# Optimization experiments

Hardware: AMD Instinct MI355X
Metric: run time of the kernel (lower is better)

The kernel has to match this reference:

```python
import math
import jax, jax.numpy as jnp
import numpy as np

B, S, D, H = 2, 2048, 2048, 16
HD = D // H
SCALE = 1.0 / math.sqrt(HD)


def setup_inputs() -> dict:
    key = jax.random.key(0)
    kx, kq, kk, kv, ko = jax.random.split(key, 5)
    w_std = 1.0 / math.sqrt(D)
    return {
        "x": jax.random.normal(kx, (B, S, D), jnp.float32),
        "Wq": jax.random.normal(kq, (D, D), jnp.float32) * w_std,
        "Wk": jax.random.normal(kk, (D, D), jnp.float32) * w_std,
        "Wv": jax.random.normal(kv, (D, D), jnp.float32) * w_std,
        "Wo": jax.random.normal(ko, (D, D), jnp.float32) * w_std,
        "attention_mask": jnp.ones((B, S), jnp.int32),
        "sliding_window": 512,
        "sink_tokens": 4,
    }


def reference(x, Wq, Wk, Wv, Wo, attention_mask, sliding_window, sink_tokens):
    b, s, d = x.shape
    # nn.Linear(bias=False): y = x @ W^T
    q = (x @ Wq.T).reshape(b, s, H, HD).transpose(0, 2, 1, 3)  # [b,h,s,hd]
    k = (x @ Wk.T).reshape(b, s, H, HD).transpose(0, 2, 1, 3)
    v = (x @ Wv.T).reshape(b, s, H, HD).transpose(0, 2, 1, 3)

    scores = jnp.einsum("bhqd,bhkd->bhqk", q, k) * SCALE  # [b,h,s,s]

    i = jnp.arange(s)[:, None]
    j = jnp.arange(s)[None, :]
    causal = j <= i
    window = (j >= i - sliding_window + 1) & (j <= i)
    # sink mask in the source fills [0:i+1] for every row (rows < sink_tokens
    # and rows >= sink_tokens alike), i.e. it is identical to the causal mask.
    sink = causal
    allowed = causal & window & sink  # [s,s]
    pad = (attention_mask != 0)[:, None, None, :]  # [b,1,1,s]
    scores = jnp.where(allowed[None, None] & pad, scores, -jnp.inf)

    attn = jax.nn.softmax(scores, axis=-1)
    out = jnp.einsum("bhqk,bhkd->bhqd", attn, v)  # [b,h,s,hd]
    out = out.transpose(0, 2, 1, 3).reshape(b, s, d)
    return out @ Wo.T
```

## Files before the change

kernel.cpp:

```cpp
#include <hip/hip_runtime.h>
#include <stdint.h>


typedef __attribute__((ext_vector_type(8))) short short8;
typedef __attribute__((ext_vector_type(4))) float f32x4;

#define DEV static __device__ __forceinline__

DEV unsigned short f2bf(float f) {
  unsigned u = __builtin_bit_cast(unsigned, f);
  u += 0x7fffu + ((u >> 16) & 1u);
  return (unsigned short)(u >> 16);
}

DEV void async16(const void* g, void* l) {
  __builtin_amdgcn_global_load_lds(
      (const __attribute__((address_space(1))) unsigned int*)g,
      (__attribute__((address_space(3))) unsigned int*)l, 16, 0, 0);
}

__global__ void cast_bf16(const float* __restrict__ src,
                          unsigned short* __restrict__ dst, int n8) {
  int i = blockIdx.x * blockDim.x + threadIdx.x;
  if (i >= n8) return;
  const float4* s4 = (const float4*)src;
  float4 a = s4[2 * (size_t)i], b = s4[2 * (size_t)i + 1];
  short8 o;
  o[0] = (short)f2bf(a.x); o[1] = (short)f2bf(a.y);
  o[2] = (short)f2bf(a.z); o[3] = (short)f2bf(a.w);
  o[4] = (short)f2bf(b.x); o[5] = (short)f2bf(b.y);
  o[6] = (short)f2bf(b.z); o[7] = (short)f2bf(b.w);
  *(short8*)(dst + 8 * (size_t)i) = o;
}

constexpr int GK = 2048, GN = 2048;

template <bool STORE_BF16>
__global__ __launch_bounds__(256) void gemm_bt(
    const unsigned short* __restrict__ A, const unsigned short* __restrict__ B,
    void* __restrict__ Cout, size_t obuf_stride) {
  __shared__ short As[128 * 32];
  __shared__ short Bs[128 * 32];
  const int t = threadIdx.x;
  const int wave = t >> 6, lane = t & 63;
  const int row0 = blockIdx.x * 128;
  const int col0g = blockIdx.y * 128;
  const int nb = col0g >> 11, col0 = col0g & 2047;
  const int wrow = (wave >> 1) * 64, wcol = (wave & 1) * 64;

  f32x4 acc[4][4] = {};

  const int srow = wave * 16 + (lane >> 2);
  const int cg = (lane & 3) ^ (lane >> 4);
  const unsigned short* Ag0 = A + (size_t)(row0 + srow) * GK + cg * 8;
  const unsigned short* Ag1 = A + (size_t)(row0 + 64 + srow) * GK + cg * 8;
  const unsigned short* Bg0 = B + (size_t)(col0g + srow) * GK + cg * 8;
  const unsigned short* Bg1 = B + (size_t)(col0g + 64 + srow) * GK + cg * 8;
  char* lA0 = (char*)As + wave * 1024;
  char* lA1 = (char*)As + 4096 + wave * 1024;
  char* lB0 = (char*)Bs + wave * 1024;
  char* lB1 = (char*)Bs + 4096 + wave * 1024;

  const int quad = lane >> 4, l15 = lane & 15;
  const int cpos = quad ^ ((l15 >> 2) & 3);
  const short* ap[4];
  const short* bp[4];
#pragma unroll
  for (int i = 0; i < 4; ++i) {
    ap[i] = As + (wrow + i * 16 + l15) * 32 + cpos * 8;
    bp[i] = Bs + (wcol + i * 16 + l15) * 32 + cpos * 8;
  }

  for (int kk = 0; kk < GK; kk += 32) {
    async16(Ag0 + kk, lA0);
    async16(Ag1 + kk, lA1);
    async16(Bg0 + kk, lB0);
    async16(Bg1 + kk, lB1);
    __syncthreads();
    short8 af[4], bf[4];
#pragma unroll
    for (int i = 0; i < 4; ++i) af[i] = *(const short8*)ap[i];
#pragma unroll
    for (int i = 0; i < 4; ++i) bf[i] = *(const short8*)bp[i];
#pragma unroll
    for (int mi = 0; mi < 4; ++mi)
#pragma unroll
      for (int ni = 0; ni < 4; ++ni)
        acc[mi][ni] = __builtin_amdgcn_mfma_f32_16x16x32_bf16(
            af[mi], bf[ni], acc[mi][ni], 0, 0, 0);
    __syncthreads();
  }

#pragma unroll
  for (int mi = 0; mi < 4; ++mi)
#pragma unroll
    for (int ni = 0; ni < 4; ++ni)
#pragma unroll
      for (int r = 0; r < 4; ++r) {
        int row = row0 + wrow + mi * 16 + quad * 4 + r;
        int col = col0 + wcol + ni * 16 + l15;
        if (STORE_BF16)
          ((unsigned short*)Cout)[nb * obuf_stride + (size_t)row * GN + col] =
              f2bf(acc[mi][ni][r]);
        else
          ((float*)Cout)[nb * obuf_stride + (size_t)row * GN + col] =
              acc[mi][ni][r];
      }
}

__global__ __launch_bounds__(256) void transpose_v(
    const unsigned short* __restrict__ vb, unsigned short* __restrict__ vtb) {
  __shared__ unsigned short tile[64][72];
  const int s0 = blockIdx.x * 64, d0 = blockIdx.y * 64, b = blockIdx.z;
  const int tid = threadIdx.x;
  const int c8 = tid & 7;
#pragma unroll
  for (int i = 0; i < 2; ++i) {
    int row = i * 32 + (tid >> 3);
    uint4 v = *(const uint4*)(vb + (size_t)(b * 2048 + s0 + row) * 2048 + d0 + c8 * 8);
    *(uint4*)&tile[row][c8 * 8] = v;
  }
  __syncthreads();
#pragma unroll
  for (int i = 0; i < 2; ++i) {
    int dr = i * 32 + (tid >> 3);
    short8 sv;
#pragma unroll
    for (int j = 0; j < 8; ++j) sv[j] = (short)tile[c8 * 8 + j][dr];
    int d = d0 + dr;
    int h = d >> 7, hd = d & 127;
    *(short8*)(vtb + ((size_t)(b * 16 + h) * 128 + hd) * 2048 + s0 + c8 * 8) = sv;
  }
}

__global__ __launch_bounds__(256, 2) void attn_mfma(
    const unsigned short* __restrict__ Qm, const unsigned short* __restrict__ Km,
    const unsigned short* __restrict__ Vt, unsigned short* __restrict__ Om,
    const int* __restrict__ amask, const int* __restrict__ winp) {
  constexpr int S = 2048, D = 2048, HD = 128;
  const float SCALE = 0.08838834764831845f;

  __shared__ short Ks[64 * 128];
  __shared__ short Vts[128 * 64];
  __shared__ short Ps[4][2][16 * 64];

  const int t = threadIdx.x, w = t >> 6, lane = t & 63;
  const int quad = lane >> 4, l15 = lane & 15;
  const int l7 = l15 & 7;
  const int qt = blockIdx.x, h = blockIdx.y, b = blockIdx.z;
  const int qi0 = qt * 128;
  const int win = winp[0];

  short8 qf[2][4];
#pragma unroll
  for (int mi = 0; mi < 2; ++mi) {
    const unsigned short* qp =
        Qm + (size_t)(b * S + qi0 + w * 32 + mi * 16 + l15) * D + h * HD + quad * 8;
#pragma unroll
    for (int kc = 0; kc < 4; ++kc) qf[mi][kc] = *(const short8*)(qp + kc * 32);
  }

  f32x4 o[2][8] = {};
  float m_r[2][4], l_r[2][4];
#pragma unroll
  for (int mi = 0; mi < 2; ++mi)
#pragma unroll
    for (int r = 0; r < 4; ++r) { m_r[mi][r] = -1e30f; l_r[mi][r] = 0.f; }

  int lowj = qi0 - win + 1;
  if (lowj < 0) lowj = 0;
  const int jt0 = lowj >> 6, jt1 = 2 * qt + 1;

  const int gmin = qi0 + w * 32, gmax = gmin + 31;
  const int krow = lane >> 4, kpos = lane & 15;
  const int vrow = lane >> 3, vpos = lane & 7;

  for (int jt = jt0; jt <= jt1; ++jt) {
    const int j0 = jt * 64;
    __syncthreads();
#pragma unroll
    for (int ii = 0; ii < 4; ++ii) {
      int row = ii * 16 + w * 4 + krow;
      int c = kpos ^ (row & 7);
      async16(Km + (size_t)(b * S + j0 + row) * D + h * HD + c * 8,
              (char*)Ks + (ii * 16 + w * 4) * 256);
    }
#pragma unroll
    for (int ii = 0; ii < 4; ++ii) {
      int row = ii * 32 + w * 8 + vrow;
      int c = vpos ^ (row & 7);
      async16(Vt + ((size_t)(b * 16 + h) * 128 + row) * S + j0 + c * 8,
              (char*)Vts + (ii * 32 + w * 8) * 128);
    }
    __syncthreads();

    if (j0 > gmax || j0 + 63 < gmin - win + 1) continue;

    int amv[4];
#pragma unroll
    for (int ni = 0; ni < 4; ++ni) amv[ni] = amask[b * S + j0 + ni * 16 + l15];

    f32x4 sS[2][4];
#pragma unroll
    for (int ni = 0; ni < 4; ++ni) {
      f32x4 a0 = {0.f, 0.f, 0.f, 0.f}, a1 = {0.f, 0.f, 0.f, 0.f};
#pragma unroll
      for (int kc = 0; kc < 4; ++kc) {
        int pos = (kc * 4 + quad) ^ l7;
        short8 bk = *(const short8*)&Ks[(ni * 16 + l15) * 128 + pos * 8];
        a0 = __builtin_amdgcn_mfma_f32_16x16x32_bf16(qf[0][kc], bk, a0, 0, 0, 0);
        a1 = __builtin_amdgcn_mfma_f32_16x16x32_bf16(qf[1][kc], bk, a1, 0, 0, 0);
      }
      sS[0][ni] = a0;
      sS[1][ni] = a1;
    }

    float alpha[2][4];
#pragma unroll
    for (int mi = 0; mi < 2; ++mi) {
      float sv[4][4];
#pragma unroll
      for (int ni = 0; ni < 4; ++ni)
#pragma unroll
        for (int r = 0; r < 4; ++r) {
          int gi = qi0 + w * 32 + mi * 16 + quad * 4 + r;
          int gj = j0 + ni * 16 + l15;
          bool ok = (gj <= gi) && (gj >= gi - win + 1) && (amv[ni] != 0);
          sv[ni][r] = ok ? sS[mi][ni][r] * SCALE : -1e30f;
        }
      float mnew[4];
#pragma unroll
      for (int r = 0; r < 4; ++r) {
        float mx = fmaxf(fmaxf(sv[0][r], sv[1][r]), fmaxf(sv[2][r], sv[3][r]));
        mx = fmaxf(mx, __shfl_xor(mx, 1));
        mx = fmaxf(mx, __shfl_xor(mx, 2));
        mx = fmaxf(mx, __shfl_xor(mx, 4));
        mx = fmaxf(mx, __shfl_xor(mx, 8));
        float mn = fmaxf(m_r[mi][r], mx);
        alpha[mi][r] = __expf(m_r[mi][r] - mn);
        m_r[mi][r] = mn;
        mnew[r] = mn;
      }
      float rs[4] = {0.f, 0.f, 0.f, 0.f};
#pragma unroll
      for (int ni = 0; ni < 4; ++ni)
#pragma unroll
        for (int r = 0; r < 4; ++r) {
          float p = (sv[ni][r] > -1e29f) ? __expf(sv[ni][r] - mnew[r]) : 0.f;
          sv[ni][r] = p;
          rs[r] += p;
        }
#pragma unroll
      for (int r = 0; r < 4; ++r) {
        float s = rs[r];
        s += __shfl_xor(s, 1);
        s += __shfl_xor(s, 2);
        s += __shfl_xor(s, 4);
        s += __shfl_xor(s, 8);
        l_r[mi][r] = l_r[mi][r] * alpha[mi][r] + s;
      }
#pragma unroll
      for (int ni = 0; ni < 4; ++ni)
#pragma unroll
        for (int r = 0; r < 4; ++r) {
          int row = quad * 4 + r;
          int col = ni * 16 + l15;
          int pos = (col >> 3) ^ (row & 7);
          Ps[w][mi][row * 64 + pos * 8 + (col & 7)] = (short)f2bf(sv[ni][r]);
        }
    }
#pragma unroll
    for (int mi = 0; mi < 2; ++mi)
#pragma unroll
      for (int ni2 = 0; ni2 < 8; ++ni2)
#pragma unroll
        for (int r = 0; r < 4; ++r) o[mi][ni2][r] *= alpha[mi][r];

    __asm__ __volatile__("s_waitcnt lgkmcnt(0)" ::: "memory");

    short8 aP[2][2];
#pragma unroll
    for (int mi = 0; mi < 2; ++mi)
#pragma unroll
      for (int kc2 = 0; kc2 < 2; ++kc2) {
        int pos = (kc2 * 4 + quad) ^ l7;
        aP[mi][kc2] = *(const short8*)&Ps[w][mi][l15 * 64 + pos * 8];
      }
#pragma unroll
    for (int ni2 = 0; ni2 < 8; ++ni2)
#pragma unroll
      for (int kc2 = 0; kc2 < 2; ++kc2) {
        int pos = (kc2 * 4 + quad) ^ l7;
        short8 bv = *(const short8*)&Vts[(ni2 * 16 + l15) * 64 + pos * 8];
        o[0][ni2] = __builtin_amdgcn_mfma_f32_16x16x32_bf16(aP[0][kc2], bv,
                                                            o[0][ni2], 0, 0, 0);
        o[1][ni2] = __builtin_amdgcn_mfma_f32_16x16x32_bf16(aP[1][kc2], bv,
                                                            o[1][ni2], 0, 0, 0);
      }
  }

#pragma unroll
  for (int mi = 0; mi < 2; ++mi) {
    float inv[4];
#pragma unroll
    for (int r = 0; r < 4; ++r) inv[r] = 1.f / l_r[mi][r];
#pragma unroll
    for (int ni2 = 0; ni2 < 8; ++ni2)
#pragma unroll
      for (int r = 0; r < 4; ++r) {
        int row = qi0 + w * 32 + mi * 16 + quad * 4 + r;
        Om[(size_t)(b * S + row) * D + h * HD + ni2 * 16 + l15] =
            f2bf(o[mi][ni2][r] * inv[r]);
      }
  }
}

extern "C" void kernel_launch(void* const* d_in, const int* in_sizes, int n_in,
                              void* d_out, int out_size, void* d_ws,
                              size_t ws_size, hipStream_t stream) {
  (void)in_sizes; (void)n_in; (void)out_size; (void)ws_size;
  const float* x  = (const float*)d_in[0];
  const float* Wq = (const float*)d_in[1];
  const float* Wk = (const float*)d_in[2];
  const float* Wv = (const float*)d_in[3];
  const float* Wo = (const float*)d_in[4];
  const int* am   = (const int*)d_in[5];
  const int* win  = (const int*)d_in[6];

  char* ws = (char*)d_ws;
  unsigned short* xb   = (unsigned short*)(ws + 0);
  unsigned short* vtb  = (unsigned short*)(ws + 0);
  unsigned short* wqkv = (unsigned short*)(ws + 16777216);
  unsigned short* wob  = (unsigned short*)(ws + 41943040);
  unsigned short* qb   = (unsigned short*)(ws + 50331648);
  unsigned short* kb   = (unsigned short*)(ws + 67108864);
  unsigned short* vb   = (unsigned short*)(ws + 83886080);
  unsigned short* ab   = (unsigned short*)(ws + 100663296);

  cast_bf16<<<dim3(4096), dim3(256), 0, stream>>>(x, xb, 1048576);
  cast_bf16<<<dim3(2048), dim3(256), 0, stream>>>(Wq, wqkv, 524288);
  cast_bf16<<<dim3(2048), dim3(256), 0, stream>>>(Wk, wqkv + 4194304, 524288);
  cast_bf16<<<dim3(2048), dim3(256), 0, stream>>>(Wv, wqkv + 8388608, 524288);
  cast_bf16<<<dim3(2048), dim3(256), 0, stream>>>(Wo, wob, 524288);

  gemm_bt<true><<<dim3(32, 48), dim3(256), 0, stream>>>(xb, wqkv, qb, 8388608);

  transpose_v<<<dim3(32, 32, 2), dim3(256), 0, stream>>>(vb, vtb);

  attn_mfma<<<dim3(16, 16, 2), dim3(256), 0, stream>>>(qb, kb, vtb, ab, am, win);

  gemm_bt<false><<<dim3(32, 16), dim3(256), 0, stream>>>(ab, wob, d_out, 0);
}
```

Baseline: 378.6 us.

## Fuse cast kernels and split-K the output projection with atomics

Merges the five fp32-to-bf16 cast launches into a single kernel that picks its source and destination from the block index, cutting launch overhead. The output projection GEMM now splits K into two halves across blockIdx.z and accumulates into a zeroed fp32 output with atomicAdd, doubling the block count from 512 to 1024 to better fill the GPU. This adds a memset and atomic traffic, and the summation order becomes nondeterministic.

```diff
diff --git a/kernel.cpp b/kernel.cpp
--- a/kernel.cpp
+++ b/kernel.cpp
@@ -19,10 +19,26 @@
       (__attribute__((address_space(3))) unsigned int*)l, 16, 0, 0);
 }
 
-__global__ void cast_bf16(const float* __restrict__ src,
-                          unsigned short* __restrict__ dst, int n8) {
-  int i = blockIdx.x * blockDim.x + threadIdx.x;
-  if (i >= n8) return;
+__global__ __launch_bounds__(256) void cast_all(
+    const float* __restrict__ x, const float* __restrict__ Wq,
+    const float* __restrict__ Wk, const float* __restrict__ Wv,
+    const float* __restrict__ Wo, unsigned short* __restrict__ xb,
+    unsigned short* __restrict__ wqkv, unsigned short* __restrict__ wob) {
+  const int bid = blockIdx.x;
+  const float* src;
+  unsigned short* dst;
+  int i;
+  if (bid < 4096) {
+    src = x; dst = xb; i = bid * 256 + threadIdx.x;
+  } else if (bid < 6144) {
+    src = Wq; dst = wqkv; i = (bid - 4096) * 256 + threadIdx.x;
+  } else if (bid < 8192) {
+    src = Wk; dst = wqkv + 4194304; i = (bid - 6144) * 256 + threadIdx.x;
+  } else if (bid < 10240) {
+    src = Wv; dst = wqkv + 8388608; i = (bid - 8192) * 256 + threadIdx.x;
+  } else {
+    src = Wo; dst = wob; i = (bid - 10240) * 256 + threadIdx.x;
+  }
   const float4* s4 = (const float4*)src;
   float4 a = s4[2 * (size_t)i], b = s4[2 * (size_t)i + 1];
   short8 o;
@@ -35,10 +51,9 @@
 
 constexpr int GK = 2048, GN = 2048;
 
-template <bool STORE_BF16>
 __global__ __launch_bounds__(256) void gemm_bt(
     const unsigned short* __restrict__ A, const unsigned short* __restrict__ B,
-    void* __restrict__ Cout, size_t obuf_stride) {
+    unsigned short* __restrict__ Cout, size_t obuf_stride) {
   __shared__ short As[128 * 32];
   __shared__ short Bs[128 * 32];
   const int t = threadIdx.x;
@@ -99,12 +114,73 @@
       for (int r = 0; r < 4; ++r) {
         int row = row0 + wrow + mi * 16 + quad * 4 + r;
         int col = col0 + wcol + ni * 16 + l15;
-        if (STORE_BF16)
-          ((unsigned short*)Cout)[nb * obuf_stride + (size_t)row * GN + col] =
-              f2bf(acc[mi][ni][r]);
-        else
-          ((float*)Cout)[nb * obuf_stride + (size_t)row * GN + col] =
-              acc[mi][ni][r];
+        Cout[nb * obuf_stride + (size_t)row * GN + col] = f2bf(acc[mi][ni][r]);
+      }
+}
+
+__global__ __launch_bounds__(256) void gemm_sk(
+    const unsigned short* __restrict__ A, const unsigned short* __restrict__ B,
+    float* __restrict__ Cout) {
+  __shared__ short As[128 * 32];
+  __shared__ short Bs[128 * 32];
+  const int t = threadIdx.x;
+  const int wave = t >> 6, lane = t & 63;
+  const int row0 = blockIdx.x * 128, col0 = blockIdx.y * 128;
+  const int k0 = blockIdx.z * 1024;
+  const int wrow = (wave >> 1) * 64, wcol = (wave & 1) * 64;
+
+  f32x4 acc[4][4] = {};
+
+  const int srow = wave * 16 + (lane >> 2);
+  const int cg = (lane & 3) ^ (lane >> 4);
+  const unsigned short* Ag0 = A + (size_t)(row0 + srow) * GK + cg * 8;
+  const unsigned short* Ag1 = A + (size_t)(row0 + 64 + srow) * GK + cg * 8;
+  const unsigned short* Bg0 = B + (size_t)(col0 + srow) * GK + cg * 8;
+  const unsigned short* Bg1 = B + (size_t)(col0 + 64 + srow) * GK + cg * 8;
+  char* lA0 = (char*)As + wave * 1024;
+  char* lA1 = (char*)As + 4096 + wave * 1024;
+  char* lB0 = (char*)Bs + wave * 1024;
+  char* lB1 = (char*)Bs + 4096 + wave * 1024;
+
+  const int quad = lane >> 4, l15 = lane & 15;
+  const int cpos = quad ^ ((l15 >> 2) & 3);
+  const short* ap[4];
+  const short* bp[4];
+#pragma unroll
+  for (int i = 0; i < 4; ++i) {
+    ap[i] = As + (wrow + i * 16 + l15) * 32 + cpos * 8;
+    bp[i] = Bs + (wcol + i * 16 + l15) * 32 + cpos * 8;
+  }
+
+  for (int kk = k0; kk < k0 + 1024; kk += 32) {
+    async16(Ag0 + kk, lA0);
+    async16(Ag1 + kk, lA1);
+    async16(Bg0 + kk, lB0);
+    async16(Bg1 + kk, lB1);
+    __syncthreads();
+    short8 af[4], bf[4];
+#pragma unroll
+    for (int i = 0; i < 4; ++i) af[i] = *(const short8*)ap[i];
+#pragma unroll
+    for (int i = 0; i < 4; ++i) bf[i] = *(const short8*)bp[i];
+#pragma unroll
+    for (int mi = 0; mi < 4; ++mi)
+#pragma unroll
+      for (int ni = 0; ni < 4; ++ni)
+        acc[mi][ni] = __builtin_amdgcn_mfma_f32_16x16x32_bf16(
+            af[mi], bf[ni], acc[mi][ni], 0, 0, 0);
+    __syncthreads();
+  }
+
+#pragma unroll
+  for (int mi = 0; mi < 4; ++mi)
+#pragma unroll
+    for (int ni = 0; ni < 4; ++ni)
+#pragma unroll
+      for (int r = 0; r < 4; ++r) {
+        int row = row0 + wrow + mi * 16 + quad * 4 + r;
+        int col = col0 + wcol + ni * 16 + l15;
+        atomicAdd(&Cout[(size_t)row * GN + col], acc[mi][ni][r]);
       }
 }
 
@@ -333,21 +409,19 @@
   unsigned short* wqkv = (unsigned short*)(ws + 16777216);
   unsigned short* wob  = (unsigned short*)(ws + 41943040);
   unsigned short* qb   = (unsigned short*)(ws + 50331648);
-  unsigned short* kb   = (unsigned short*)(ws + 67108864);
   unsigned short* vb   = (unsigned short*)(ws + 83886080);
   unsigned short* ab   = (unsigned short*)(ws + 100663296);
 
-  cast_bf16<<<dim3(4096), dim3(256), 0, stream>>>(x, xb, 1048576);
-  cast_bf16<<<dim3(2048), dim3(256), 0, stream>>>(Wq, wqkv, 524288);
-  cast_bf16<<<dim3(2048), dim3(256), 0, stream>>>(Wk, wqkv + 4194304, 524288);
-  cast_bf16<<<dim3(2048), dim3(256), 0, stream>>>(Wv, wqkv + 8388608, 524288);
-  cast_bf16<<<dim3(2048), dim3(256), 0, stream>>>(Wo, wob, 524288);
-
-  gemm_bt<true><<<dim3(32, 48), dim3(256), 0, stream>>>(xb, wqkv, qb, 8388608);
+  hipMemsetAsync(d_out, 0, (size_t)out_size * sizeof(float), stream);
+
+  cast_all<<<dim3(12288), dim3(256), 0, stream>>>(x, Wq, Wk, Wv, Wo, xb, wqkv, wob);
+
+  gemm_bt<<<dim3(32, 48), dim3(256), 0, stream>>>(xb, wqkv, qb, 8388608);
 
   transpose_v<<<dim3(32, 32, 2), dim3(256), 0, stream>>>(vb, vtb);
 
-  attn_mfma<<<dim3(16, 16, 2), dim3(256), 0, stream>>>(qb, kb, vtb, ab, am, win);
-
-  gemm_bt<false><<<dim3(32, 16), dim3(256), 0, stream>>>(ab, wob, d_out, 0);
-}
+  attn_mfma<<<dim3(16, 16, 2), dim3(256), 0, stream>>>(qb, qb + 8388608, vtb,
+                                                       ab, am, win);
+
+  gemm_sk<<<dim3(32, 16, 2), dim3(256), 0, stream>>>(ab, wob, (float*)d_out);
+}
```

After: 418.9 us. +10.6%, slower.
